# Performance work log

Measured on AMD Instinct MI355X. Metric: run time of the kernel, lower is better.

The kernel has to match this reference:

```python
import jax, jax.numpy as jnp
import numpy as np

N = 100000
C = 128
H = 8
D = C // H  # head_dim = 16
E = 640000


def setup_inputs() -> dict:
    key = jax.random.key(0)
    ks = jax.random.split(key, 10)
    s = 1.0 / np.sqrt(C)
    return {
        "features": jax.random.normal(ks[0], (N, C), dtype=jnp.float32),
        "edge_index": jax.random.randint(ks[1], (2, E), 0, N, dtype=jnp.int64),
        "Wq": jax.random.uniform(ks[2], (C, C), jnp.float32, -s, s),
        "bq": jnp.zeros((C,), jnp.float32),
        "Wk": jax.random.uniform(ks[3], (C, C), jnp.float32, -s, s),
        "bk": jnp.zeros((C,), jnp.float32),
        "Wv": jax.random.uniform(ks[4], (C, C), jnp.float32, -s, s),
        "bv": jnp.zeros((C,), jnp.float32),
        "Wo": jax.random.uniform(ks[5], (C, C), jnp.float32, -s, s),
        "bo": jnp.zeros((C,), jnp.float32),
    }


def reference(features, edge_index, Wq, bq, Wk, bk, Wv, bv, Wo, bo):
    row, col = edge_index[0], edge_index[1]  # [E], [E]
    # Linear projections (torch Linear: x @ W.T + b), reshape to heads
    q = (features @ Wq.T + bq).reshape(N, H, D)
    k = (features @ Wk.T + bk).reshape(N, H, D)
    v = (features @ Wv.T + bv).reshape(N, H, D)
    # Per-edge dot-product scores [E, H]
    attn = jnp.einsum('ehd,ehd->eh', q[row], k[col]) / jnp.sqrt(jnp.float32(D))
    # Faithful to original: softmax over ALL edges (dim=0), per head
    attn = jax.nn.softmax(attn, axis=0)
    # Weighted scatter-add of source values into destination nodes
    msgs = attn[:, :, None] * v[col]  # [E, H, D]
    out = jax.ops.segment_sum(msgs, row, num_segments=N)  # [N, H, D]
    out = out.reshape(N, C)
    return out @ Wo.T + bo
```

## Files before the change

kernel.cpp:

```cpp
#include <hip/hip_runtime.h>


#define TPB 256

typedef __attribute__((ext_vector_type(8))) short short8;
typedef __attribute__((ext_vector_type(4))) short short4v;
typedef __attribute__((ext_vector_type(4))) float f32x4;

__device__ __forceinline__ short f2bf(float f) {
    unsigned u = __float_as_uint(f);
    u += 0x7fffu + ((u >> 16) & 1u);
    return (short)(u >> 16);
}
__device__ __forceinline__ float bf2f(short s) {
    return __uint_as_float(((unsigned)(unsigned short)s) << 16);
}

template<bool IN_BF16, bool OUT_BF16>
__device__ __forceinline__ void gemm_body(
    const void* __restrict__ Xv, int nrows,
    const short* __restrict__ Wb, const float* __restrict__ bias,
    void* __restrict__ Yv, int xblk)
{
    __shared__ short lw[16384];
    const int tid = threadIdx.x;

    #pragma unroll
    for (int r = 0; r < 8; ++r) {
        int c = r * 256 + tid;
        int fragid = c >> 6, ln = c & 63;
        int n = fragid >> 2, kc = fragid & 3;
        const short* gsrc = &Wb[(n*16 + (ln & 15))*128 + kc*32 + (ln >> 4)*8];
        __builtin_amdgcn_global_load_lds(
            (const __attribute__((address_space(1))) void*)gsrc,
            (__attribute__((address_space(3))) void*)&lw[c * 8],
            16, 0, 0);
    }

    const int wid = tid >> 6;
    const int lane = tid & 63;
    const int l15 = lane & 15;
    const int lh  = lane >> 4;
    const int rowbase = xblk * 128 + wid * 32;
    const int r0 = rowbase + l15, r1 = r0 + 16;
    const bool vv0 = r0 < nrows, vv1 = r1 < nrows;

    short8 xfr[4][2];
    if (IN_BF16) {
        const short* Xb = (const short*)Xv;
        #pragma unroll
        for (int kc = 0; kc < 4; ++kc) {
            xfr[kc][0] = vv0 ? *(const short8*)&Xb[(size_t)r0*128 + kc*32 + lh*8]
                             : (short8)(short)0;
            xfr[kc][1] = vv1 ? *(const short8*)&Xb[(size_t)r1*128 + kc*32 + lh*8]
                             : (short8)(short)0;
        }
    } else {
        const float* Xf = (const float*)Xv;
        const float4* P0 = (const float4*)(Xf + (size_t)r0 * 128);
        const float4* P1 = (const float4*)(Xf + (size_t)r1 * 128);
        float4 xa[4][2], xb[4][2];
        #pragma unroll
        for (int kc = 0; kc < 4; ++kc) {
            xa[kc][0] = vv0 ? P0[kc*8 + lh*2]     : make_float4(0.f,0.f,0.f,0.f);
            xb[kc][0] = vv0 ? P0[kc*8 + lh*2 + 1] : make_float4(0.f,0.f,0.f,0.f);
            xa[kc][1] = vv1 ? P1[kc*8 + lh*2]     : make_float4(0.f,0.f,0.f,0.f);
            xb[kc][1] = vv1 ? P1[kc*8 + lh*2 + 1] : make_float4(0.f,0.f,0.f,0.f);
        }
        #pragma unroll
        for (int kc = 0; kc < 4; ++kc)
            #pragma unroll
            for (int g = 0; g < 2; ++g) {
                xfr[kc][g][0] = f2bf(xa[kc][g].x);
                xfr[kc][g][1] = f2bf(xa[kc][g].y);
                xfr[kc][g][2] = f2bf(xa[kc][g].z);
                xfr[kc][g][3] = f2bf(xa[kc][g].w);
                xfr[kc][g][4] = f2bf(xb[kc][g].x);
                xfr[kc][g][5] = f2bf(xb[kc][g].y);
                xfr[kc][g][6] = f2bf(xb[kc][g].z);
                xfr[kc][g][7] = f2bf(xb[kc][g].w);
            }
    }

    __syncthreads();

    f32x4 acc[8][2];
    #pragma unroll
    for (int n = 0; n < 8; ++n) { acc[n][0] = (f32x4)0.f; acc[n][1] = (f32x4)0.f; }

    #pragma unroll
    for (int kc = 0; kc < 4; ++kc) {
        short8 wf[8];
        #pragma unroll
        for (int n = 0; n < 8; ++n)
            wf[n] = *(const short8*)&lw[((n*4 + kc)*64 + lane) * 8];
        #pragma unroll
        for (int n = 0; n < 8; ++n) {
            acc[n][0] = __builtin_amdgcn_mfma_f32_16x16x32_bf16(wf[n], xfr[kc][0], acc[n][0], 0, 0, 0);
            acc[n][1] = __builtin_amdgcn_mfma_f32_16x16x32_bf16(wf[n], xfr[kc][1], acc[n][1], 0, 0, 0);
        }
    }

    #pragma unroll
    for (int g = 0; g < 2; ++g) {
        int row = rowbase + g*16 + l15;
        if (row >= nrows) continue;
        #pragma unroll
        for (int n = 0; n < 8; ++n) {
            float4 b4 = *(const float4*)&bias[n*16 + lh*4];
            float y0 = acc[n][g][0] + b4.x;
            float y1 = acc[n][g][1] + b4.y;
            float y2 = acc[n][g][2] + b4.z;
            float y3 = acc[n][g][3] + b4.w;
            if (OUT_BF16) {
                short4v s; s[0]=f2bf(y0); s[1]=f2bf(y1); s[2]=f2bf(y2); s[3]=f2bf(y3);
                *(short4v*)&((short*)Yv)[(size_t)row * 128 + n*16 + lh*4] = s;
            } else {
                *(float4*)&((float*)Yv)[(size_t)row * 128 + n*16 + lh*4] =
                    make_float4(y0, y1, y2, y3);
            }
        }
    }
}

__global__ __launch_bounds__(256) void gemm_out_kernel(
    const short* __restrict__ Xb, int nrows,
    const short* __restrict__ Wb, const float* __restrict__ bias,
    float* __restrict__ Y)
{
    gemm_body<true, false>(Xb, nrows, Wb, bias, Y, blockIdx.x);
}

__global__ __launch_bounds__(256) void gemm_qkv_kernel(
    const float* __restrict__ X, int nrows, int nxblk,
    const short* __restrict__ WB,
    const float* __restrict__ bq, const float* __restrict__ bk,
    const float* __restrict__ bv,
    short* __restrict__ Yb, size_t slice)
{
    int b = blockIdx.x;
    int k = b & 7, j = b >> 3;
    int jd = j / 3, w = j - 3 * jd;
    int x = k + 8 * jd;
    if (x >= nxblk) return;
    const float* bias = (w == 0) ? bq : (w == 1) ? bk : bv;
    gemm_body<false, true>(X, nrows, WB + w * 16384, bias,
                           Yb + (size_t)w * slice, x);
}

__global__ void init_kernel(int* __restrict__ deg, int n,
                            const int* __restrict__ raw, int* __restrict__ flag)
{
    int i = blockIdx.x * TPB + threadIdx.x;
    if (i < n) deg[i] = 0;
    if (blockIdx.x == 0 && threadIdx.x == 0) {
        int odd_nonzero = 0;
        for (int k = 0; k < 128; ++k)
            if (raw[2 * k + 1] != 0) odd_nonzero = 1;
        *flag = odd_nonzero ? 0 : 1;
    }
}

__global__ void conv_hist_wconv_kernel(
    const void* __restrict__ raw, int E, const int* __restrict__ flag,
    int* __restrict__ out, int* __restrict__ deg, int ebC,
    const float* __restrict__ W0, const float* __restrict__ W1,
    const float* __restrict__ W2, const float* __restrict__ W3,
    short* __restrict__ WB)
{
    int b = blockIdx.x;
    if (b < ebC) {
        int i = b * TPB + threadIdx.x;
        if (i >= 2 * E) return;
        int v;
        if (*flag) v = (int)((const long long*)raw)[i];
        else       v = ((const int*)raw)[i];
        out[i] = v;
        if (i < E) atomicAdd(&deg[v], 1);
    } else {
        int i = (b - ebC) * TPB + threadIdx.x;
        if (i >= 65536) return;
        const float* W = (i < 16384) ? W0 : (i < 32768) ? W1 : (i < 49152) ? W2 : W3;
        WB[i] = f2bf(W[i & 16383]);
    }
}

__global__ void scan1_kernel(const int* __restrict__ deg, int n,
                             int* __restrict__ rowstart, int* __restrict__ bsum)
{
    __shared__ int sm[TPB];
    int t = threadIdx.x;
    int gid = blockIdx.x * TPB + t;
    int v = (gid < n) ? deg[gid] : 0;
    sm[t] = v;
    __syncthreads();
    for (int off = 1; off < TPB; off <<= 1) {
        int x = (t >= off) ? sm[t - off] : 0;
        __syncthreads();
        sm[t] += x;
        __syncthreads();
    }
    if (gid < n) rowstart[gid] = sm[t] - v;
    if (t == TPB - 1) bsum[blockIdx.x] = sm[t];
}

__global__ void scan2_kernel(int* __restrict__ bsum, int nb)
{
    __shared__ int sm[512];
    int t = threadIdx.x;
    int v = (t < nb) ? bsum[t] : 0;
    sm[t] = v;
    __syncthreads();
    for (int off = 1; off < 512; off <<= 1) {
        int x = (t >= off) ? sm[t - off] : 0;
        __syncthreads();
        sm[t] += x;
        __syncthreads();
    }
    if (t < nb) bsum[t] = sm[t] - v;
}

__global__ void scan3_kernel(int* __restrict__ rowstart, int* __restrict__ cursor,
                             int n, int E, const int* __restrict__ bsum)
{
    int gid = blockIdx.x * TPB + threadIdx.x;
    if (gid < n) {
        int v = rowstart[gid] + bsum[blockIdx.x];
        rowstart[gid] = v;
        cursor[gid] = v;
    }
    if (gid == 0) rowstart[n] = E;
}

__global__ void fill_kernel(const int* __restrict__ ei, int E,
                            int* __restrict__ cursor,
                            int* __restrict__ ecol, int* __restrict__ erow)
{
    int e = blockIdx.x * TPB + threadIdx.x;
    if (e >= E) return;
    int r = ei[e];
    int pos = atomicAdd(&cursor[r], 1);
    ecol[pos] = ei[E + e];
    erow[pos] = r;
}

__global__ __launch_bounds__(256) void epar_score_stats_kernel(
    const short* __restrict__ Qb, const short* __restrict__ Kb,
    const int* __restrict__ erow, const int* __restrict__ ecol, int EH,
    float* __restrict__ S, float* __restrict__ mpart, float* __restrict__ zpart)
{
    int t = threadIdx.x;
    int stride = gridDim.x * TPB;
    float m = -3.0e38f, z = 0.f;
    for (int idx = blockIdx.x * TPB + t; idx < EH; idx += stride) {
        int p = idx >> 3, h = idx & 7;
        int r = erow[p], c = ecol[p];
        const short8* q8 = (const short8*)(Qb + (size_t)r * 128 + h * 16);
        const short8* k8 = (const short8*)(Kb + (size_t)c * 128 + h * 16);
        short8 q0 = q8[0], q1 = q8[1], k0 = k8[0], k1 = k8[1];
        float dot = 0.f;
        #pragma unroll
        for (int i = 0; i < 8; ++i) {
            dot += bf2f(q0[i]) * bf2f(k0[i]);
            dot += bf2f(q1[i]) * bf2f(k1[i]);
        }
        float s = dot * 0.25f;
        S[idx] = s;
        float M = fmaxf(m, s);
        z = z * __expf(m - M) + __expf(s - M);
        m = M;
    }
    __shared__ float sm[TPB], sz[TPB];
    sm[t] = m; sz[t] = z;
    __syncthreads();
    for (int off = 128; off >= 8; off >>= 1) {
        if (t < off) {
            float m2 = sm[t + off], z2 = sz[t + off];
            float M = fmaxf(sm[t], m2);
            sz[t] = sz[t] * __expf(sm[t] - M) + z2 * __expf(m2 - M);
            sm[t] = M;
        }
        __syncthreads();
    }
    if (t < 8) {
        mpart[blockIdx.x * 8 + t] = sm[t];
        zpart[blockIdx.x * 8 + t] = sz[t];
    }
}

__global__ void stats_reduce_kernel(const float* __restrict__ mpart,
                                    const float* __restrict__ zpart,
                                    int nb, float* __restrict__ MZ)
{
    int t = threadIdx.x;
    int h = t & 7, chunk = t >> 3;
    float m = -3.0e38f, z = 0.f;
    for (int i = chunk; i < nb; i += 32) {
        float m2 = mpart[i * 8 + h], z2 = zpart[i * 8 + h];
        float M = fmaxf(m, m2);
        z = z * __expf(m - M) + z2 * __expf(m2 - M);
        m = M;
    }
    __shared__ float sm[TPB], sz[TPB];
    sm[t] = m; sz[t] = z;
    __syncthreads();
    for (int off = 128; off >= 8; off >>= 1) {
        if (t < off) {
            float m2 = sm[t + off], z2 = sz[t + off];
            float M = fmaxf(sm[t], m2);
            sz[t] = sz[t] * __expf(sm[t] - M) + z2 * __expf(m2 - M);
            sm[t] = M;
        }
        __syncthreads();
    }
    if (t < 8) { MZ[t] = sm[t]; MZ[8 + t] = sz[t]; }
}

__global__ __launch_bounds__(256) void gather_kernel(
    const float* __restrict__ S, const short* __restrict__ Vb,
    const int* __restrict__ ecol,
    const int* __restrict__ rowstart,
    const float* __restrict__ MZ, int N,
    short* __restrict__ outb)
{
    int idx = blockIdx.x * TPB + threadIdx.x;
    if (idx >= N * 8) return;
    int node = idx >> 3, h = idx & 7;
    float M = MZ[h];
    float invZ = 1.0f / MZ[8 + h];
    int p0 = rowstart[node], p1 = rowstart[node + 1];

    float a[16];
    #pragma unroll
    for (int i = 0; i < 16; ++i) a[i] = 0.f;

    if (p0 < p1) {
        short8 va0, va1, vb0, vb1;
        float sa, sb;
        {
            const short8* vp = (const short8*)(Vb + (size_t)ecol[p0] * 128 + h * 16);
            va0 = vp[0]; va1 = vp[1];
            sa = S[(size_t)p0 * 8 + h];
        }
        if (p0 + 1 < p1) {
            const short8* vp = (const short8*)(Vb + (size_t)ecol[p0+1] * 128 + h * 16);
            vb0 = vp[0]; vb1 = vp[1];
            sb = S[(size_t)(p0+1) * 8 + h];
        } else { vb0 = va0; vb1 = va1; sb = sa; }

        for (int p = p0; p < p1; ++p) {
            short8 vc0 = vb0, vc1 = vb1;
            float sc = sb;
            if (p + 2 < p1) {
                const short8* vp = (const short8*)(Vb + (size_t)ecol[p+2] * 128 + h * 16);
                vc0 = vp[0]; vc1 = vp[1];
                sc = S[(size_t)(p+2) * 8 + h];
            }
            float w = __expf(sa - M) * invZ;
            #pragma unroll
            for (int i = 0; i < 8; ++i) {
                a[i]     += w * bf2f(va0[i]);
                a[8 + i] += w * bf2f(va1[i]);
            }
            va0 = vb0; va1 = vb1; vb0 = vc0; vb1 = vc1;
            sa = sb; sb = sc;
        }
    }
    short8 o0, o1;
    #pragma unroll
    for (int i = 0; i < 8; ++i) { o0[i] = f2bf(a[i]); o1[i] = f2bf(a[8 + i]); }
    short8* ob = (short8*)(outb + (size_t)node * 128 + h * 16);
    ob[0] = o0; ob[1] = o1;
}

extern "C" void kernel_launch(void* const* d_in, const int* in_sizes, int n_in,
                              void* d_out, int out_size, void* d_ws, size_t ws_size,
                              hipStream_t stream)
{
    const float* feat = (const float*)d_in[0];
    const void*  eraw = d_in[1];
    const float* Wq = (const float*)d_in[2];
    const float* bq = (const float*)d_in[3];
    const float* Wk = (const float*)d_in[4];
    const float* bk = (const float*)d_in[5];
    const float* Wv = (const float*)d_in[6];
    const float* bv = (const float*)d_in[7];
    const float* Wo = (const float*)d_in[8];
    const float* bo = (const float*)d_in[9];

    const int N = in_sizes[0] / 128;
    const int E = in_sizes[1] / 2;
    const size_t NC = (size_t)N * 128;
    const int EH = E * 8;
    const int gbN = (N * 8 + TPB - 1) / TPB;
    const int EG  = 2500;

    short* Qb   = (short*)d_ws;
    short* Kb   = Qb + NC;
    short* Vb   = Kb + NC;
    short* ACCb = Vb + NC;
    float* S    = (float*)(ACCb + NC);
    int*   EI   = (int*)(S + EH);
    short* WB   = (short*)(EI + 2 * E);
    float* mpart = (float*)(WB + 65536);
    float* zpart = mpart + (size_t)EG * 8;
    float* MZ    = zpart + (size_t)EG * 8;
    int*   flag  = (int*)(MZ + 16);
    int* deg      = flag + 16;
    int* rowstart = deg + N;
    int* cursor   = rowstart + N + 1;
    int* bsum     = cursor + N;
    int* ecol     = bsum + 512;
    int* erow     = ecol + E;

    const int nbS = (N + TPB - 1) / TPB;
    const int ebE = (E + TPB - 1) / TPB;
    const int ebC = (2 * E + TPB - 1) / TPB;

    init_kernel<<<nbS, TPB, 0, stream>>>(deg, N, (const int*)eraw, flag);
    conv_hist_wconv_kernel<<<ebC + 256, TPB, 0, stream>>>(
        eraw, E, flag, EI, deg, ebC, Wq, Wk, Wv, Wo, WB);
    scan1_kernel<<<nbS, TPB, 0, stream>>>(deg, N, rowstart, bsum);
    scan2_kernel<<<1, 512, 0, stream>>>(bsum, nbS);
    scan3_kernel<<<nbS, TPB, 0, stream>>>(rowstart, cursor, N, E, bsum);
    fill_kernel<<<ebE, TPB, 0, stream>>>(EI, E, cursor, ecol, erow);

    const int gb = (N + 127) / 128;
    const int qkvgrid = 8 * 3 * ((gb + 7) / 8);
    gemm_qkv_kernel<<<qkvgrid, TPB, 0, stream>>>(feat, N, gb, WB, bq, bk, bv, Qb, NC);

    epar_score_stats_kernel<<<EG, TPB, 0, stream>>>(Qb, Kb, erow, ecol, EH,
                                                    S, mpart, zpart);
    stats_reduce_kernel<<<1, TPB, 0, stream>>>(mpart, zpart, EG, MZ);

    gather_kernel<<<gbN, TPB, 0, stream>>>(S, Vb, ecol, rowstart, MZ, N, ACCb);

    gemm_out_kernel<<<gb, TPB, 0, stream>>>(ACCb, N, WB + 3 * 16384, bo, (float*)d_out);
}
```

Baseline: 247.9 us.

## Sort nodes by degree to balance per-wave work in gather kernel

Builds a degree histogram during the scan, prefix-sums it in a small kernel, then fills a node permutation grouped by in-degree bucket. The gather kernel walks nodes in this permuted order so threads in a wave handle rows of similar length, which is meant to cut divergence and idle lanes in the per-node edge loop. The cost is two extra kernel launches, heavily contended atomics on a few histogram bins, and less locality in the gather's rowstart reads and output writes.

```diff
diff --git a/kernel.cpp b/kernel.cpp
--- a/kernel.cpp
+++ b/kernel.cpp
@@ -149,10 +149,12 @@
 }
 
 __global__ void init_kernel(int* __restrict__ deg, int n,
+                            int* __restrict__ dbin,
                             const int* __restrict__ raw, int* __restrict__ flag)
 {
     int i = blockIdx.x * TPB + threadIdx.x;
     if (i < n) deg[i] = 0;
+    if (blockIdx.x == 0 && threadIdx.x < 64) dbin[threadIdx.x] = 0;
     if (blockIdx.x == 0 && threadIdx.x == 0) {
         int odd_nonzero = 0;
         for (int k = 0; k < 128; ++k)
@@ -186,12 +188,14 @@
 }
 
 __global__ void scan1_kernel(const int* __restrict__ deg, int n,
-                             int* __restrict__ rowstart, int* __restrict__ bsum)
+                             int* __restrict__ rowstart, int* __restrict__ bsum,
+                             int* __restrict__ dbin)
 {
     __shared__ int sm[TPB];
     int t = threadIdx.x;
     int gid = blockIdx.x * TPB + t;
     int v = (gid < n) ? deg[gid] : 0;
+    if (gid < n) atomicAdd(&dbin[v < 63 ? v : 63], 1);
     sm[t] = v;
     __syncthreads();
     for (int off = 1; off < TPB; off <<= 1) {
@@ -230,6 +234,32 @@
         cursor[gid] = v;
     }
     if (gid == 0) rowstart[n] = E;
+}
+
+__global__ void scan_deg_kernel(const int* __restrict__ dbin, int* __restrict__ dcur)
+{
+    __shared__ int sm[64];
+    int t = threadIdx.x;
+    int v = dbin[t];
+    sm[t] = v;
+    __syncthreads();
+    for (int off = 1; off < 64; off <<= 1) {
+        int x = (t >= off) ? sm[t - off] : 0;
+        __syncthreads();
+        sm[t] += x;
+        __syncthreads();
+    }
+    dcur[t] = sm[t] - v;
+}
+
+__global__ void fill_perm_kernel(const int* __restrict__ deg, int n,
+                                 int* __restrict__ dcur, int* __restrict__ nodeperm)
+{
+    int i = blockIdx.x * TPB + threadIdx.x;
+    if (i >= n) return;
+    int d = deg[i];
+    int pos = atomicAdd(&dcur[d < 63 ? d : 63], 1);
+    nodeperm[pos] = i;
 }
 
 __global__ void fill_kernel(const int* __restrict__ ei, int E,
@@ -320,12 +350,14 @@
     const float* __restrict__ S, const short* __restrict__ Vb,
     const int* __restrict__ ecol,
     const int* __restrict__ rowstart,
+    const int* __restrict__ nodeperm,
     const float* __restrict__ MZ, int N,
     short* __restrict__ outb)
 {
     int idx = blockIdx.x * TPB + threadIdx.x;
     if (idx >= N * 8) return;
-    int node = idx >> 3, h = idx & 7;
+    int node = nodeperm[idx >> 3];
+    int h = idx & 7;
     float M = MZ[h];
     float invZ = 1.0f / MZ[8 + h];
     int p0 = rowstart[node], p1 = rowstart[node + 1];
@@ -412,18 +444,23 @@
     int* bsum     = cursor + N;
     int* ecol     = bsum + 512;
     int* erow     = ecol + E;
+    int* dbin     = erow + E;
+    int* dcur     = dbin + 64;
+    int* nodeperm = dcur + 64;
 
     const int nbS = (N + TPB - 1) / TPB;
     const int ebE = (E + TPB - 1) / TPB;
     const int ebC = (2 * E + TPB - 1) / TPB;
 
-    init_kernel<<<nbS, TPB, 0, stream>>>(deg, N, (const int*)eraw, flag);
+    init_kernel<<<nbS, TPB, 0, stream>>>(deg, N, dbin, (const int*)eraw, flag);
     conv_hist_wconv_kernel<<<ebC + 256, TPB, 0, stream>>>(
         eraw, E, flag, EI, deg, ebC, Wq, Wk, Wv, Wo, WB);
-    scan1_kernel<<<nbS, TPB, 0, stream>>>(deg, N, rowstart, bsum);
+    scan1_kernel<<<nbS, TPB, 0, stream>>>(deg, N, rowstart, bsum, dbin);
     scan2_kernel<<<1, 512, 0, stream>>>(bsum, nbS);
     scan3_kernel<<<nbS, TPB, 0, stream>>>(rowstart, cursor, N, E, bsum);
+    scan_deg_kernel<<<1, 64, 0, stream>>>(dbin, dcur);
     fill_kernel<<<ebE, TPB, 0, stream>>>(EI, E, cursor, ecol, erow);
+    fill_perm_kernel<<<nbS, TPB, 0, stream>>>(deg, N, dcur, nodeperm);
 
     const int gb = (N + 127) / 128;
     const int qkvgrid = 8 * 3 * ((gb + 7) / 8);
@@ -433,7 +470,8 @@
                                                     S, mpart, zpart);
     stats_reduce_kernel<<<1, TPB, 0, stream>>>(mpart, zpart, EG, MZ);
 
-    gather_kernel<<<gbN, TPB, 0, stream>>>(S, Vb, ecol, rowstart, MZ, N, ACCb);
+    gather_kernel<<<gbN, TPB, 0, stream>>>(S, Vb, ecol, rowstart, nodeperm,
+                                           MZ, N, ACCb);
 
     gemm_out_kernel<<<gb, TPB, 0, stream>>>(ACCb, N, WB + 3 * 16384, bo, (float*)d_out);
 }
```

Result: slower. 967.4 us (+290.2%).
